# Performance work log

Hardware: AMD Instinct MI355X
Metric: run time of the kernel (lower is better)

The kernel has to match this reference:

```python
import jax, jax.numpy as jnp
import numpy as np

IN_SHAPE = (8, 16, 8)     # hidden_shape, prod = 1024
FF_SHAPE = (16, 16, 16)   # ff_shape, prod = 4096
RANKS = (1, 8, 8, 1)      # tt_ranks


def _make_cores(key, in_shape, out_shape, ranks):
    cores = []
    for k in range(3):
        key, sub = jax.random.split(key)
        shape = (ranks[k], in_shape[k], out_shape[k], ranks[k + 1])
        # glorot-ish scale per core
        scale = (2.0 / (in_shape[k] * ranks[k] + out_shape[k] * ranks[k + 1])) ** 0.5
        cores.append(jax.random.normal(sub, shape, dtype=jnp.float32) * scale)
    return key, cores


def setup_inputs() -> dict:
    key = jax.random.key(0)
    key, kx = jax.random.split(key)
    x = jax.random.normal(kx, (8192, int(np.prod(IN_SHAPE))), dtype=jnp.float32)
    key, c0 = _make_cores(key, IN_SHAPE, FF_SHAPE, RANKS)
    key, c1 = _make_cores(key, FF_SHAPE, IN_SHAPE, RANKS)
    b0 = jnp.zeros((int(np.prod(FF_SHAPE)),), dtype=jnp.float32)
    b1 = jnp.zeros((int(np.prod(IN_SHAPE)),), dtype=jnp.float32)
    return {
        "x": x,
        "c0a": c0[0], "c0b": c0[1], "c0c": c0[2], "b0": b0,
        "c1a": c1[0], "c1b": c1[1], "c1c": c1[2], "b1": b1,
    }


def tt_linear(x, cores, bias, in_shape, out_shape):
    # x: (B, prod(in_shape)); cores[k]: (r_k, in_k, out_k, r_{k+1})
    B = x.shape[0]
    t = x.reshape(B, *in_shape)                      # (B, i, j, k)
    t = jnp.einsum('bijk,aior->bjkor', t, cores[0])  # (B, j, k, o1, r1)
    t = jnp.einsum('bjkor,rjps->bkops', t, cores[1]) # (B, k, o1, o2, r2)
    t = jnp.einsum('bkops,skqu->bopq', t, cores[2])  # (B, o1, o2, o3)
    return t.reshape(B, -1) + bias


def reference(x, c0a, c0b, c0c, b0, c1a, c1b, c1c, b1):
    h = tt_linear(x, (c0a, c0b, c0c), b0, IN_SHAPE, FF_SHAPE)
    h = jax.nn.gelu(h, approximate=False)  # nn.GELU default = exact erf form
    out = tt_linear(h, (c1a, c1b, c1c), b1, FF_SHAPE, IN_SHAPE)
    return out
```

## Files before the change

kernel.cpp:

```cpp
#include <hip/hip_runtime.h>
#include <math.h>

typedef _Float16 f16x8 __attribute__((ext_vector_type(8)));
typedef _Float16 f16x4 __attribute__((ext_vector_type(4)));
typedef float f32x4 __attribute__((ext_vector_type(4)));

__device__ __forceinline__ void async_copy16(const void* g, void* l) {
    __builtin_amdgcn_global_load_lds(
        (const __attribute__((address_space(1))) void*)g,
        (__attribute__((address_space(3))) void*)l, 16, 0, 0);
}

__global__ __launch_bounds__(256) void cast_f32_f16_kernel(
    const float4* __restrict__ in, f16x4* __restrict__ out) {
    int i = blockIdx.x * 256 + threadIdx.x;
    float4 v = in[i];
    f16x4 o;
    o[0] = (_Float16)v.x; o[1] = (_Float16)v.y;
    o[2] = (_Float16)v.z; o[3] = (_Float16)v.w;
    out[i] = o;
}

__global__ __launch_bounds__(256) void build_E0_kernel(
    const float* __restrict__ c0b, const float* __restrict__ c0c, float* __restrict__ E0) {
    int idx = blockIdx.x * 256 + threadIdx.x;
    int q = idx & 15, k = (idx >> 4) & 7, p = (idx >> 7) & 15, j = (idx >> 11) & 15, r = idx >> 15;
    float s = 0.f;
#pragma unroll
    for (int ss = 0; ss < 8; ++ss)
        s += c0b[((r * 16 + j) * 16 + p) * 8 + ss] * c0c[(ss * 8 + k) * 16 + q];
    E0[idx] = s;
}

__global__ __launch_bounds__(256) void build_E1_kernel(
    const float* __restrict__ c1b, const float* __restrict__ c1c, float* __restrict__ E1) {
    int idx = blockIdx.x * 256 + threadIdx.x;
    int q = idx & 7, k = (idx >> 3) & 15, p = (idx >> 7) & 15, j = (idx >> 11) & 15, r = idx >> 15;
    float s = 0.f;
#pragma unroll
    for (int ss = 0; ss < 8; ++ss)
        s += c1b[((r * 16 + j) * 16 + p) * 8 + ss] * c1c[(ss * 16 + k) * 8 + q];
    E1[idx] = s;
}

__global__ __launch_bounds__(256) void build_W0t_v2(
    const float* __restrict__ c0a, const float* __restrict__ E0, _Float16* __restrict__ W0t) {
    const int j = blockIdx.x >> 4, p = blockIdx.x & 15;
    const int t = threadIdx.x;
    const int q = t & 15, k = (t >> 4) & 7, ih = t >> 7;
    float e[8];
#pragma unroll
    for (int r = 0; r < 8; ++r)
        e[r] = E0[(((r * 16 + j) * 16 + p) * 8 + k) * 16 + q];
#pragma unroll
    for (int ii = 0; ii < 4; ++ii) {
        const int i = ih * 4 + ii;
#pragma unroll
        for (int o = 0; o < 16; ++o) {
            float s = 0.f;
#pragma unroll
            for (int r = 0; r < 8; ++r) s += c0a[(i * 16 + o) * 8 + r] * e[r];
            W0t[(size_t)((o * 16 + p) * 16 + q) * 1024 + (i * 128 + j * 8 + k)] = (_Float16)s;
        }
    }
}

__global__ __launch_bounds__(256) void build_W1t_v2(
    const float* __restrict__ c1a, const float* __restrict__ E1, _Float16* __restrict__ W1t) {
    const int j = blockIdx.x >> 4, p = blockIdx.x & 15;
    const int t = threadIdx.x;
    const int q = t & 7, k = (t >> 3) & 15, ih = t >> 7;
    float e[8];
#pragma unroll
    for (int r = 0; r < 8; ++r)
        e[r] = E1[(((r * 16 + j) * 16 + p) * 16 + k) * 8 + q];
#pragma unroll
    for (int ii = 0; ii < 8; ++ii) {
        const int i = ih * 8 + ii;
#pragma unroll
        for (int o = 0; o < 8; ++o) {
            float s = 0.f;
#pragma unroll
            for (int r = 0; r < 8; ++r) s += c1a[(i * 8 + o) * 8 + r] * e[r];
            W1t[(size_t)((o * 16 + p) * 8 + q) * 4096 + (i * 16 + j) * 16 + k] = (_Float16)s;
        }
    }
}

template <int OUTMODE>
__global__ __launch_bounds__(256) void gemm_bt_kernel(
    const _Float16* __restrict__ A, const _Float16* __restrict__ Bt,
    const float* __restrict__ bias, void* __restrict__ Cout,
    int M, int N, int K) {
    constexpr int BK = 32;
    __shared__ alignas(16) _Float16 sA[128 * BK];
    __shared__ alignas(16) _Float16 sB[128 * BK];

    const int t = threadIdx.x;
    const int lane = t & 63;
    const int w = t >> 6;
    const int m0 = blockIdx.x * 128;
    const int n0 = blockIdx.y * 128;
    const int wm = (w & 1) * 64;
    const int wn = (w >> 1) * 64;
    const int lm = lane & 15;
    const int lq = lane >> 4;
    const int kxor = lq ^ ((lm >> 1) & 3);

    f32x4 acc[4][4] = {};

    const int srow = t >> 2;
    const int sk = ((t & 3) ^ ((t >> 3) & 3)) * 8;
    const _Float16* gA = A + (size_t)(m0 + srow) * K + sk;
    const _Float16* gB = Bt + (size_t)(n0 + srow) * K + sk;
    _Float16* lA = sA + srow * BK + (t & 3) * 8;
    _Float16* lB = sB + srow * BK + (t & 3) * 8;
    const size_t rowskip = (size_t)64 * K;

    for (int k0 = 0; k0 < K; k0 += BK) {
        async_copy16(gA + k0, lA);
        async_copy16(gA + k0 + rowskip, lA + 64 * BK);
        async_copy16(gB + k0, lB);
        async_copy16(gB + k0 + rowskip, lB + 64 * BK);
        __syncthreads();

        f16x8 af[4], bf[4];
#pragma unroll
        for (int i = 0; i < 4; ++i) {
            af[i] = *(const f16x8*)(sA + (wm + i * 16 + lm) * BK + kxor * 8);
            bf[i] = *(const f16x8*)(sB + (wn + i * 16 + lm) * BK + kxor * 8);
        }
#pragma unroll
        for (int i = 0; i < 4; ++i)
#pragma unroll
            for (int j = 0; j < 4; ++j)
                acc[i][j] = __builtin_amdgcn_mfma_f32_16x16x32_f16(af[i], bf[j], acc[i][j], 0, 0, 0);
        __syncthreads();
    }

    if (OUTMODE == 1) {
        _Float16* C = (_Float16*)Cout;
#pragma unroll
        for (int i = 0; i < 4; ++i)
#pragma unroll
            for (int j = 0; j < 4; ++j) {
                int col = n0 + wn + j * 16 + lm;
                float bv = bias[col];
#pragma unroll
                for (int r = 0; r < 4; ++r) {
                    int row = m0 + wm + i * 16 + lq * 4 + r;
                    float v = acc[i][j][r] + bv;
                    float u = v * (0.7978845608028654f + 0.0356774081363001f * v * v);
                    float e = __builtin_amdgcn_exp2f(u * 2.8853900817779268f);
                    float rc = __builtin_amdgcn_rcpf(e + 1.0f);
                    C[(size_t)row * N + col] = (_Float16)(v * (1.0f - rc));
                }
            }
    } else {
        float* C = (float*)Cout;
#pragma unroll
        for (int i = 0; i < 4; ++i)
#pragma unroll
            for (int j = 0; j < 4; ++j) {
                int col = n0 + wn + j * 16 + lm;
                float bv = bias[col];
#pragma unroll
                for (int r = 0; r < 4; ++r) {
                    int row = m0 + wm + i * 16 + lq * 4 + r;
                    C[(size_t)row * N + col] = acc[i][j][r] + bv;
                }
            }
    }
}

extern "C" void kernel_launch(void* const* d_in, const int* in_sizes, int n_in,
                              void* d_out, int out_size, void* d_ws, size_t ws_size,
                              hipStream_t stream) {
    const float* x   = (const float*)d_in[0];
    const float* c0a = (const float*)d_in[1];
    const float* c0b = (const float*)d_in[2];
    const float* c0c = (const float*)d_in[3];
    const float* b0  = (const float*)d_in[4];
    const float* c1a = (const float*)d_in[5];
    const float* c1b = (const float*)d_in[6];
    const float* c1c = (const float*)d_in[7];
    const float* b1  = (const float*)d_in[8];
    float* out = (float*)d_out;

    char* ws = (char*)d_ws;
    _Float16* xh  = (_Float16*)(ws);
    _Float16* W0t = (_Float16*)(ws + (size_t)(16u << 20));
    _Float16* W1t = (_Float16*)(ws + (size_t)(24u << 20));
    _Float16* h   = (_Float16*)(ws + (size_t)(32u << 20));
    float* E0     = (float*)(ws + (size_t)(32u << 20));
    float* E1     = (float*)(ws + (size_t)(33u << 20));

    cast_f32_f16_kernel<<<dim3(8192), dim3(256), 0, stream>>>((const float4*)x, (f16x4*)xh);
    build_E0_kernel<<<dim3(1024), dim3(256), 0, stream>>>(c0b, c0c, E0);
    build_E1_kernel<<<dim3(1024), dim3(256), 0, stream>>>(c1b, c1c, E1);
    build_W0t_v2<<<dim3(256), dim3(256), 0, stream>>>(c0a, E0, W0t);
    build_W1t_v2<<<dim3(256), dim3(256), 0, stream>>>(c1a, E1, W1t);
    gemm_bt_kernel<1><<<dim3(64, 32), dim3(256), 0, stream>>>(xh, W0t, b0, (void*)h, 8192, 4096, 1024);
    gemm_bt_kernel<0><<<dim3(64, 8), dim3(256), 0, stream>>>(h, W1t, b1, (void*)out, 8192, 1024, 4096);
}
```

Before: 309.2 us.

## Fuse TT weight builders and remap GEMM blocks by XCD for L2 locality

Merges the E-intermediate kernels into the dense-weight builders, computing the b·c core product per (o,p) tile in shared memory and writing vectorized f16x4 rows. This drops two launches and the global round trip of the E buffers. The GEMMs now use a 1D grid whose block index is remapped so consecutive blocks on the same XCD cover a compact 8x8 tile region, aiming to improve L2 reuse. It also adds a 64KB LDS footprint per builder block, which limits their occupancy.

After: 325.7 us. +5.3%, slower.

```diff
diff --git a/kernel.cpp b/kernel.cpp
--- a/kernel.cpp
+++ b/kernel.cpp
@@ -21,68 +21,87 @@
     out[i] = o;
 }
 
-__global__ __launch_bounds__(256) void build_E0_kernel(
-    const float* __restrict__ c0b, const float* __restrict__ c0c, float* __restrict__ E0) {
-    int idx = blockIdx.x * 256 + threadIdx.x;
-    int q = idx & 15, k = (idx >> 4) & 7, p = (idx >> 7) & 15, j = (idx >> 11) & 15, r = idx >> 15;
-    float s = 0.f;
-#pragma unroll
-    for (int ss = 0; ss < 8; ++ss)
-        s += c0b[((r * 16 + j) * 16 + p) * 8 + ss] * c0c[(ss * 8 + k) * 16 + q];
-    E0[idx] = s;
-}
-
-__global__ __launch_bounds__(256) void build_E1_kernel(
-    const float* __restrict__ c1b, const float* __restrict__ c1c, float* __restrict__ E1) {
-    int idx = blockIdx.x * 256 + threadIdx.x;
-    int q = idx & 7, k = (idx >> 3) & 15, p = (idx >> 7) & 15, j = (idx >> 11) & 15, r = idx >> 15;
-    float s = 0.f;
-#pragma unroll
-    for (int ss = 0; ss < 8; ++ss)
-        s += c1b[((r * 16 + j) * 16 + p) * 8 + ss] * c1c[(ss * 16 + k) * 8 + q];
-    E1[idx] = s;
-}
-
-__global__ __launch_bounds__(256) void build_W0t_v2(
-    const float* __restrict__ c0a, const float* __restrict__ E0, _Float16* __restrict__ W0t) {
-    const int j = blockIdx.x >> 4, p = blockIdx.x & 15;
+__global__ __launch_bounds__(256) void build_W0t_fused(
+    const float* __restrict__ c0a, const float* __restrict__ c0b,
+    const float* __restrict__ c0c, _Float16* __restrict__ W0t) {
+    __shared__ float G[16384];
+    const int o = blockIdx.x >> 4, p = blockIdx.x & 15;
     const int t = threadIdx.x;
-    const int q = t & 15, k = (t >> 4) & 7, ih = t >> 7;
-    float e[8];
-#pragma unroll
-    for (int r = 0; r < 8; ++r)
-        e[r] = E0[(((r * 16 + j) * 16 + p) * 8 + k) * 16 + q];
-#pragma unroll
-    for (int ii = 0; ii < 4; ++ii) {
-        const int i = ih * 4 + ii;
-#pragma unroll
-        for (int o = 0; o < 16; ++o) {
-            float s = 0.f;
-#pragma unroll
-            for (int r = 0; r < 8; ++r) s += c0a[(i * 16 + o) * 8 + r] * e[r];
-            W0t[(size_t)((o * 16 + p) * 16 + q) * 1024 + (i * 128 + j * 8 + k)] = (_Float16)s;
-        }
-    }
-}
-
-__global__ __launch_bounds__(256) void build_W1t_v2(
-    const float* __restrict__ c1a, const float* __restrict__ E1, _Float16* __restrict__ W1t) {
-    const int j = blockIdx.x >> 4, p = blockIdx.x & 15;
+#pragma unroll
+    for (int n = 0; n < 64; ++n) {
+        int idx = t + 256 * n;
+        int k = idx & 7, j = (idx >> 3) & 15, r = (idx >> 7) & 7, q = idx >> 10;
+        float s = 0.f;
+#pragma unroll
+        for (int ss = 0; ss < 8; ++ss)
+            s += c0b[((r * 16 + j) * 16 + p) * 8 + ss] * c0c[(ss * 8 + k) * 16 + q];
+        G[idx] = s;
+    }
+    __syncthreads();
+    const int i = t >> 5, j = (t >> 1) & 15, kq = t & 1;
+    float a[8];
+#pragma unroll
+    for (int r = 0; r < 8; ++r) a[r] = c0a[(i * 16 + o) * 8 + r];
+    const float4* G4 = (const float4*)G;
+#pragma unroll
+    for (int q = 0; q < 16; ++q) {
+        float4 acc = {0.f, 0.f, 0.f, 0.f};
+#pragma unroll
+        for (int r = 0; r < 8; ++r) {
+            float4 g = G4[q * 256 + r * 32 + j * 2 + kq];
+            acc.x += a[r] * g.x; acc.y += a[r] * g.y;
+            acc.z += a[r] * g.z; acc.w += a[r] * g.w;
+        }
+        f16x4 h4;
+        h4[0] = (_Float16)acc.x; h4[1] = (_Float16)acc.y;
+        h4[2] = (_Float16)acc.z; h4[3] = (_Float16)acc.w;
+        *(f16x4*)(W0t + (size_t)((o * 16 + p) * 16 + q) * 1024 + t * 4) = h4;
+    }
+}
+
+__global__ __launch_bounds__(256) void build_W1t_fused(
+    const float* __restrict__ c1a, const float* __restrict__ c1b,
+    const float* __restrict__ c1c, _Float16* __restrict__ W1t) {
+    __shared__ float G[16384];
+    const int o = blockIdx.x >> 4, p = blockIdx.x & 15;
     const int t = threadIdx.x;
-    const int q = t & 7, k = (t >> 3) & 15, ih = t >> 7;
-    float e[8];
-#pragma unroll
-    for (int r = 0; r < 8; ++r)
-        e[r] = E1[(((r * 16 + j) * 16 + p) * 16 + k) * 8 + q];
-#pragma unroll
-    for (int ii = 0; ii < 8; ++ii) {
-        const int i = ih * 8 + ii;
-#pragma unroll
-        for (int o = 0; o < 8; ++o) {
-            float s = 0.f;
-#pragma unroll
-            for (int r = 0; r < 8; ++r) s += c1a[(i * 8 + o) * 8 + r] * e[r];
-            W1t[(size_t)((o * 16 + p) * 8 + q) * 4096 + (i * 16 + j) * 16 + k] = (_Float16)s;
+#pragma unroll
+    for (int n = 0; n < 64; ++n) {
+        int idx = t + 256 * n;
+        int k = idx & 15, j = (idx >> 4) & 15, r = (idx >> 8) & 7, q = idx >> 11;
+        float s = 0.f;
+#pragma unroll
+        for (int ss = 0; ss < 8; ++ss)
+            s += c1b[((r * 16 + j) * 16 + p) * 8 + ss] * c1c[(ss * 16 + k) * 8 + q];
+        G[idx] = s;
+    }
+    __syncthreads();
+    const int ig = t >> 6, j = (t >> 2) & 15, kq = t & 3;
+    float a[4][8];
+#pragma unroll
+    for (int ii = 0; ii < 4; ++ii)
+#pragma unroll
+        for (int r = 0; r < 8; ++r) a[ii][r] = c1a[((ig * 4 + ii) * 8 + o) * 8 + r];
+    const float4* G4 = (const float4*)G;
+#pragma unroll
+    for (int q = 0; q < 8; ++q) {
+        float4 acc[4] = {{0,0,0,0},{0,0,0,0},{0,0,0,0},{0,0,0,0}};
+#pragma unroll
+        for (int r = 0; r < 8; ++r) {
+            float4 g = G4[q * 512 + r * 64 + j * 4 + kq];
+#pragma unroll
+            for (int ii = 0; ii < 4; ++ii) {
+                acc[ii].x += a[ii][r] * g.x; acc[ii].y += a[ii][r] * g.y;
+                acc[ii].z += a[ii][r] * g.z; acc[ii].w += a[ii][r] * g.w;
+            }
+        }
+        const size_t rowbase = (size_t)((o * 16 + p) * 8 + q) * 4096;
+#pragma unroll
+        for (int ii = 0; ii < 4; ++ii) {
+            f16x4 h4;
+            h4[0] = (_Float16)acc[ii].x; h4[1] = (_Float16)acc[ii].y;
+            h4[2] = (_Float16)acc[ii].z; h4[3] = (_Float16)acc[ii].w;
+            *(f16x4*)(W1t + rowbase + (ig * 4 + ii) * 256 + j * 16 + kq * 4) = h4;
         }
     }
 }
@@ -96,11 +115,14 @@
     __shared__ alignas(16) _Float16 sA[128 * BK];
     __shared__ alignas(16) _Float16 sB[128 * BK];
 
+    const int f = blockIdx.x;
+    const int xcd = f & 7, s = f >> 3, g = s >> 6, u = s & 63;
+    const int m0 = (xcd * 8 + (u >> 3)) * 128;
+    const int n0 = (g * 8 + (u & 7)) * 128;
+
     const int t = threadIdx.x;
     const int lane = t & 63;
     const int w = t >> 6;
-    const int m0 = blockIdx.x * 128;
-    const int n0 = blockIdx.y * 128;
     const int wm = (w & 1) * 64;
     const int wn = (w >> 1) * 64;
     const int lm = lane & 15;
@@ -150,8 +172,8 @@
                 for (int r = 0; r < 4; ++r) {
                     int row = m0 + wm + i * 16 + lq * 4 + r;
                     float v = acc[i][j][r] + bv;
-                    float u = v * (0.7978845608028654f + 0.0356774081363001f * v * v);
-                    float e = __builtin_amdgcn_exp2f(u * 2.8853900817779268f);
+                    float uu = v * (0.7978845608028654f + 0.0356774081363001f * v * v);
+                    float e = __builtin_amdgcn_exp2f(uu * 2.8853900817779268f);
                     float rc = __builtin_amdgcn_rcpf(e + 1.0f);
                     C[(size_t)row * N + col] = (_Float16)(v * (1.0f - rc));
                 }
@@ -192,14 +214,10 @@
     _Float16* W0t = (_Float16*)(ws + (size_t)(16u << 20));
     _Float16* W1t = (_Float16*)(ws + (size_t)(24u << 20));
     _Float16* h   = (_Float16*)(ws + (size_t)(32u << 20));
-    float* E0     = (float*)(ws + (size_t)(32u << 20));
-    float* E1     = (float*)(ws + (size_t)(33u << 20));
 
     cast_f32_f16_kernel<<<dim3(8192), dim3(256), 0, stream>>>((const float4*)x, (f16x4*)xh);
-    build_E0_kernel<<<dim3(1024), dim3(256), 0, stream>>>(c0b, c0c, E0);
-    build_E1_kernel<<<dim3(1024), dim3(256), 0, stream>>>(c1b, c1c, E1);
-    build_W0t_v2<<<dim3(256), dim3(256), 0, stream>>>(c0a, E0, W0t);
-    build_W1t_v2<<<dim3(256), dim3(256), 0, stream>>>(c1a, E1, W1t);
-    gemm_bt_kernel<1><<<dim3(64, 32), dim3(256), 0, stream>>>(xh, W0t, b0, (void*)h, 8192, 4096, 1024);
-    gemm_bt_kernel<0><<<dim3(64, 8), dim3(256), 0, stream>>>(h, W1t, b1, (void*)out, 8192, 1024, 4096);
-}
+    build_W0t_fused<<<dim3(256), dim3(256), 0, stream>>>(c0a, c0b, c0c, W0t);
+    build_W1t_fused<<<dim3(128), dim3(256), 0, stream>>>(c1a, c1b, c1c, W1t);
+    gemm_bt_kernel<1><<<dim3(2048), dim3(256), 0, stream>>>(xh, W0t, b0, (void*)h, 8192, 4096, 1024);
+    gemm_bt_kernel<0><<<dim3(512), dim3(256), 0, stream>>>(h, W1t, b1, (void*)out, 8192, 1024, 4096);
+}
```
